# Kernel optimization log

Hardware: AMD Instinct MI355X
Metric: run time of the kernel (lower is better)

Reference implementation:

```python
import jax, jax.numpy as jnp
import numpy as np

IN_DIM, HIDDEN, OUT_DIM, BRANCH = 700, 1024, 20, 4
B, T = 128, 250
VTH = 1.0
WARMUP = 0
# surrogate-gradient constants (DH-SNN ActFun_adp); only used in backward
GAMMA, LENS, SCALE, HIGHT = 0.5, 0.5, 6.0, 0.15
SQRT2PI = float(np.sqrt(2.0 * np.pi))


def _gauss(x, mu, sigma):
    return jnp.exp(-((x - mu) ** 2) / (2.0 * sigma * sigma)) / (SQRT2PI * sigma)


@jax.custom_vjp
def spike_fn(x):
    # heaviside spike with multi-gaussian surrogate gradient
    return (x > 0).astype(x.dtype)


def _spike_fwd(x):
    return spike_fn(x), x


def _spike_bwd(x, g):
    temp = (_gauss(x, 0.0, LENS) * (1.0 + HIGHT)
            - _gauss(x, LENS, SCALE * LENS) * HIGHT
            - _gauss(x, -LENS, SCALE * LENS) * HIGHT)
    return (g * temp * GAMMA,)


spike_fn.defvjp(_spike_fwd, _spike_bwd)


def _branch_mask(rng):
    # each neuron's branch j sees a random disjoint slice of the (input+recurrent) fan-in
    isz = IN_DIM + HIDDEN
    seg = isz // BRANCH
    mask = np.zeros((HIDDEN * BRANCH, isz), np.float32)
    for i in range(HIDDEN):
        perm = rng.permutation(isz)
        for j in range(BRANCH):
            mask[i * BRANCH + j, perm[j * seg:(j + 1) * seg]] = 1.0
    return mask


def setup_inputs() -> dict:
    key = jax.random.key(0)
    ks = jax.random.split(key, 8)
    isz = IN_DIM + HIDDEN
    x = jax.random.normal(ks[0], (B, T, IN_DIM), jnp.float32)
    W = jax.random.normal(ks[1], (HIDDEN * BRANCH, isz), jnp.float32) / np.float32(np.sqrt(isz))
    W = W * jnp.asarray(_branch_mask(np.random.RandomState(0)))  # apply_mask() pre-applied
    b = jnp.zeros((HIDDEN * BRANCH,), jnp.float32)
    tau_m = jax.random.uniform(ks[2], (HIDDEN,), jnp.float32, 0.0, 4.0)
    tau_n = jax.random.uniform(ks[3], (HIDDEN, BRANCH), jnp.float32, 2.0, 6.0)  # low_n/high_n
    Wr = jax.random.normal(ks[4], (OUT_DIM, HIDDEN), jnp.float32) / np.float32(np.sqrt(HIDDEN))
    br = jnp.zeros((OUT_DIM,), jnp.float32)
    tau_r = jax.random.uniform(ks[5], (OUT_DIM,), jnp.float32, 0.0, 4.0)
    mem0 = jax.random.uniform(ks[6], (B, HIDDEN), jnp.float32) * VTH  # set_neuron_state: rand*vth
    return {"x": x, "W": W, "b": b, "tau_m": tau_m, "tau_n": tau_n,
            "Wr": Wr, "br": br, "tau_r": tau_r, "mem0": mem0}


def reference(x, W, b, tau_m, tau_n, Wr, br, tau_r, mem0):
    Bsz, Tlen = x.shape[0], x.shape[1]
    beta = jax.nn.sigmoid(tau_n)      # [H, BR] dendritic branch decay
    alpha = jax.nn.sigmoid(tau_m)     # [H]     soma decay
    alpha_r = jax.nn.sigmoid(tau_r)   # [O]     readout decay
    spike0 = jnp.zeros((Bsz, HIDDEN), x.dtype)
    d0 = jnp.zeros((Bsz, HIDDEN, BRANCH), x.dtype)
    rmem0 = jnp.zeros((Bsz, OUT_DIM), x.dtype)
    acc0 = jnp.zeros((Bsz, OUT_DIM), x.dtype)

    def step(carry, inp):
        mem, spk, d_in, rmem, acc = carry
        x_t, t = inp
        k = jnp.concatenate([x_t, spk], axis=1)                 # [B, in+H]
        cur = (k @ W.T + b).reshape(Bsz, HIDDEN, BRANCH)        # branch currents
        d_in = beta * d_in + (1.0 - beta) * cur                 # dendritic integration
        l_in = d_in.sum(axis=2)                                 # [B, H]
        mem = mem * alpha + (1.0 - alpha) * l_in - VTH * spk    # soma, soft reset (R_m=1)
        spk = spike_fn(mem - VTH)
        rmem = rmem * alpha_r + (1.0 - alpha_r) * (spk @ Wr.T + br)
        acc = acc + jnp.where(t > WARMUP, jax.nn.softmax(rmem, axis=1), 0.0)
        return (mem, spk, d_in, rmem, acc), None

    xs = (jnp.swapaxes(x, 0, 1), jnp.arange(Tlen))
    (_, _, _, _, acc), _ = jax.lax.scan(step, (mem0, spike0, d0, rmem0, acc0), xs)
    return acc
```

## Files before the change

### kernel.cpp

```cpp
#include <hip/hip_runtime.h>
#include <hip/hip_bf16.h>
#include <stdint.h>


typedef short short8 __attribute__((ext_vector_type(8)));
typedef float f32x4 __attribute__((ext_vector_type(4)));

#define T_STEPS 250
#define BATCH   128
#define HID     1024
#define NCOL    4096
#define IND     700
#define ISZ     1724
#define KPAD    704
#define OUTD    20
#define WGT     256
#define UPB     5632

#define O_P1F   0
#define O_SUM   4096
#define O_CHK   8192
#define O_WST   73728
#define O_WXH   16850944
#define O_XH    22618112

#define SM_BP    0
#define SM_A2    45568
#define SM_CURL2 135680
#define SM_MTB   144896
#define SM_TOTAL 153600

#define AGENT __HIP_MEMORY_SCOPE_AGENT

__device__ __forceinline__ float sigmoidf(float x) { return 1.0f / (1.0f + expf(-x)); }

__device__ __forceinline__ unsigned ldsLd(const unsigned* p) {
    return __hip_atomic_load(p, __ATOMIC_ACQUIRE, __HIP_MEMORY_SCOPE_WORKGROUP);
}
__device__ __forceinline__ void ldsSt(unsigned* p, unsigned v) {
    __hip_atomic_store(p, v, __ATOMIC_RELEASE, __HIP_MEMORY_SCOPE_WORKGROUP);
}

__device__ __forceinline__ void dma16(const void* g, void* l) {
    __builtin_amdgcn_global_load_lds(
        (const __attribute__((address_space(1))) unsigned int*)g,
        (__attribute__((address_space(3))) unsigned int*)l, 16, 0, 0);
}

__device__ __forceinline__ float qsum4(float v) {
    union { float f; int i; } a, b;
    a.f = v; b.i = __builtin_amdgcn_mov_dpp(a.i, 0xB1, 0xF, 0xF, true); v += b.f;
    a.f = v; b.i = __builtin_amdgcn_mov_dpp(a.i, 0x4E, 0xF, 0xF, true); v += b.f;
    return v;
}

__device__ __forceinline__ short bf16bits(float v) {
    union { __hip_bfloat16 h; short s; } u;
    u.h = __float2bfloat16(v);
    return u.s;
}

__global__ __launch_bounds__(256) void prep_all(
    const float* __restrict__ x, const float* __restrict__ W,
    __hip_bfloat16* __restrict__ Xh, __hip_bfloat16* __restrict__ Wxh,
    float* __restrict__ Wst, uint64_t* __restrict__ p1f,
    uint64_t* __restrict__ sums, uint64_t* __restrict__ chunks)
{
    const int bid = blockIdx.x;
    const int tid = threadIdx.x;

    if (bid < 2048) {
        const int total = T_STEPS * 2 * UPB;
        for (int unit = bid * 256 + tid; unit < total; unit += 2048 * 256) {
            int q    = unit % UPB;
            int blk  = unit / UPB;
            int half = blk & 1, t = blk >> 1;
            int row  = q / 88, m = q % 88;
            int k8   = m ^ (row & 7);
            int b    = half * 64 + row;
            int k0   = k8 * 8;
            const float* xp = x + ((long)b * T_STEPS + t) * IND + k0;
            short8 o;
            if (k0 + 8 <= IND) {
                f32x4 v0 = *(const f32x4*)xp;
                f32x4 v1 = *(const f32x4*)(xp + 4);
                #pragma unroll
                for (int e = 0; e < 4; ++e) { o[e] = bf16bits(v0[e]); o[4 + e] = bf16bits(v1[e]); }
            } else {
                #pragma unroll
                for (int e = 0; e < 8; ++e)
                    o[e] = bf16bits((k0 + e < IND) ? xp[e] : 0.0f);
            }
            *(short8*)(Xh + (size_t)unit * 8) = o;
        }
    } else if (bid < 4096) {
        if (bid == 2048) {
            for (int i = tid; i < 512; i += 256)
                __hip_atomic_store(&p1f[i], 0ull, __ATOMIC_RELAXED, AGENT);
            for (int i = tid; i < 2 * 2 * 128; i += 256)
                __hip_atomic_store(&sums[i], 0ull, __ATOMIC_RELAXED, AGENT);
            for (int i = tid; i < 2 * 2 * 128 * 16; i += 256)
                __hip_atomic_store(&chunks[i], 0ull, __ATOMIC_RELAXED, AGENT);
        }
        const int total = NCOL * 88;
        for (int unit = (bid - 2048) * 256 + tid; unit < total; unit += 2048 * 256) {
            int n = unit / 88, m = unit % 88;
            int k0 = m * 8;
            const float* wp = W + (long)n * ISZ + k0;
            short8 o;
            if (k0 + 8 <= IND) {
                f32x4 v0 = *(const f32x4*)wp;
                f32x4 v1 = *(const f32x4*)(wp + 4);
                #pragma unroll
                for (int e = 0; e < 4; ++e) { o[e] = bf16bits(v0[e]); o[4 + e] = bf16bits(v1[e]); }
            } else {
                #pragma unroll
                for (int e = 0; e < 8; ++e)
                    o[e] = bf16bits((k0 + e < IND) ? wp[e] : 0.0f);
            }
            *(short8*)(Wxh + (long)n * KPAD + k0) = o;
        }
    } else {
        __shared__ float tile[32][33];
        const int idx = bid - 4096;
        const int h0 = (idx & 31) * 32, n0 = (idx >> 5) * 32;
        const int tx = tid & 31, ty = tid >> 5;
        #pragma unroll
        for (int j = 0; j < 32; j += 8)
            tile[ty + j][tx] = W[(long)(n0 + ty + j) * ISZ + IND + h0 + tx];
        __syncthreads();
        #pragma unroll
        for (int j = 0; j < 32; j += 8)
            Wst[(long)(h0 + ty + j) * NCOL + n0 + tx] = tile[tx][ty + j];
    }
}

__global__ __launch_bounds__(256, 2) void p1_scan(
    const __hip_bfloat16* __restrict__ Xh, const __hip_bfloat16* __restrict__ Wxh,
    const float* __restrict__ bvec, const float* __restrict__ tau_m,
    const float* __restrict__ tau_n, const float* __restrict__ mem0,
    uint64_t* __restrict__ p1f)
{
    __shared__ __align__(16) uint8_t Abuf[2][22528];
    __shared__ __align__(16) float preg[2][8 * 256];
    __shared__ unsigned anySpkF;

    const int wg    = blockIdx.x;
    const int rtile = wg & 7;
    const int ctile = wg >> 3;
    const int tid   = threadIdx.x;
    const int lane  = tid & 63, wid = tid >> 6;
    const int colA  = lane & 15, kb8 = (lane >> 4) * 8;
    const int cg    = wid >> 1;
    const int p     = wid & 1;

    if (tid == 0) anySpkF = 0u;

    const int colG0 = ctile * 64 + cg * 32 + colA;
    const int colG1 = colG0 + 16;
    const int rowB  = rtile * 16 + (lane >> 4) * 4;
    float bt_[2], omb_[2], bias_[2], al_[2], oma_[2], dn[2][4], mem_[2][4];
    {
        const int cG[2] = {colG0, colG1};
        #pragma unroll
        for (int i = 0; i < 2; ++i) {
            bt_[i]   = sigmoidf(tau_n[cG[i]]);
            omb_[i]  = 1.0f - bt_[i];
            bias_[i] = bvec[cG[i]];
            al_[i]   = sigmoidf(tau_m[cG[i] >> 2]);
            oma_[i]  = 1.0f - al_[i];
            #pragma unroll
            for (int j = 0; j < 4; ++j) {
                dn[i][j]   = 0.0f;
                mem_[i][j] = mem0[(rowB + j) * HID + (cG[i] >> 2)];
            }
        }
    }

    short8 Breg[22];
    #pragma unroll
    for (int j = 0; j < 11; ++j) {
        Breg[2 * j]     = *(const short8*)(Wxh + (long)colG0 * KPAD + (11 * p + j) * 32 + kb8);
        Breg[2 * j + 1] = *(const short8*)(Wxh + (long)colG1 * KPAD + (11 * p + j) * 32 + kb8);
    }
    asm volatile("s_waitcnt vmcnt(0)" ::: "memory");
    __builtin_amdgcn_sched_barrier(0);
    #pragma unroll
    for (int i = 0; i < 22; ++i) asm volatile("" : "+v"(Breg[i]));

    const size_t sliceBase = (size_t)(rtile >> 2) * 90112 + (size_t)(rtile & 3) * 22528;
    const int dstart = (wid < 2) ? wid * 6 : 12 + (wid - 2) * 5;
    const int dcnt   = (wid < 2) ? 6 : 5;
    const char* XhB  = (const char*)Xh;

    #define ISSUE_A(T, BUF)                                                            \
        do {                                                                           \
            const char* _g = XhB + sliceBase + (size_t)(T) * 180224;                   \
            _Pragma("unroll")                                                          \
            for (int _i = 0; _i < 6; ++_i)                                             \
                if (_i < dcnt)                                                         \
                    dma16(_g + (size_t)(dstart + _i) * 1024 + (size_t)lane * 16,       \
                          (BUF) + (dstart + _i) * 1024);                               \
        } while (0)

    const int rl = lane & 15;
    const int sw = rl & 7;

    #define MFMA_BLOCK(AB, A0, A1)                                                             \
        do {                                                                                   \
            _Pragma("unroll")                                                                  \
            for (int _j = 0; _j < 11; ++_j) {                                                  \
                int _k8 = (11 * p + _j) * 4 + (lane >> 4);                                     \
                short8 _a = *(const short8*)((AB) + ((rl * 88 + (_k8 ^ sw)) << 4));            \
                A0 = __builtin_amdgcn_mfma_f32_16x16x32_bf16(_a, Breg[2 * _j],     A0, 0,0,0); \
                A1 = __builtin_amdgcn_mfma_f32_16x16x32_bf16(_a, Breg[2 * _j + 1], A1, 0,0,0); \
            }                                                                                  \
        } while (0)

    #define UPDATE_STEP(CS0, CS1)                                                  \
        do {                                                                       \
            _Pragma("unroll")                                                      \
            for (int _j = 0; _j < 4; ++_j) {                                       \
                float _d0 = bt_[0] * dn[0][_j] + omb_[0] * ((CS0)[_j] + bias_[0]); \
                float _d1 = bt_[1] * dn[1][_j] + omb_[1] * ((CS1)[_j] + bias_[1]); \
                dn[0][_j] = _d0; dn[1][_j] = _d1;                                  \
                float _l0 = qsum4(_d0), _l1 = qsum4(_d1);                          \
                float _m0 = al_[0] * mem_[0][_j] + oma_[0] * _l0;                  \
                float _m1 = al_[1] * mem_[1][_j] + oma_[1] * _l1;                  \
                mem_[0][_j] = _m0; mem_[1][_j] = _m1;                              \
                memmax = fmaxf(memmax, fmaxf(_m0, _m1));                           \
            }                                                                      \
        } while (0)

    float memmax = -1e30f;
    f32x4 own0, own1, prt0, prt1;
    const int wrSlot = (cg * 2 + (1 - p)) * 2;
    const int rdSlot = (cg * 2 + p) * 2;

    ISSUE_A(0, Abuf[0]);
    asm volatile("s_waitcnt vmcnt(0)" ::: "memory");
    __builtin_amdgcn_sched_barrier(0);
    __syncthreads();

    {
        ISSUE_A(1, Abuf[1]);
        f32x4 acc0 = {0,0,0,0}, acc1 = {0,0,0,0};
        MFMA_BLOCK(Abuf[0], acc0, acc1);
        float* wq = &preg[0][wrSlot * 256 + lane * 4];
        *(f32x4*)wq = acc0; *(f32x4*)(wq + 256) = acc1;
        asm volatile("s_waitcnt vmcnt(0) lgkmcnt(0)" ::: "memory");
        __builtin_amdgcn_sched_barrier(0);
        __builtin_amdgcn_s_barrier();
        const float* rq = &preg[0][rdSlot * 256 + lane * 4];
        prt0 = *(const f32x4*)rq; prt1 = *(const f32x4*)(rq + 256);
        own0 = acc0; own1 = acc1;
    }

    for (int t = 1; t < T_STEPS; ++t) {
        if (t + 1 < T_STEPS)
            ISSUE_A(t + 1, Abuf[(t + 1) & 1]);
        f32x4 acc0 = {0,0,0,0}, acc1 = {0,0,0,0};
        MFMA_BLOCK(Abuf[t & 1], acc0, acc1);
        {
            f32x4 cs0 = own0 + prt0;
            f32x4 cs1 = own1 + prt1;
            UPDATE_STEP(cs0, cs1);
        }
        float* wq = &preg[t & 1][wrSlot * 256 + lane * 4];
        *(f32x4*)wq = acc0; *(f32x4*)(wq + 256) = acc1;
        asm volatile("s_waitcnt vmcnt(0) lgkmcnt(0)" ::: "memory");
        __builtin_amdgcn_sched_barrier(0);
        __builtin_amdgcn_s_barrier();
        const float* rq = &preg[t & 1][rdSlot * 256 + lane * 4];
        prt0 = *(const f32x4*)rq; prt1 = *(const f32x4*)(rq + 256);
        own0 = acc0; own1 = acc1;
    }

    {
        f32x4 cs0 = own0 + prt0;
        f32x4 cs1 = own1 + prt1;
        UPDATE_STEP(cs0, cs1);
    }

    if (__any(memmax > 1.0f) && lane == 0) anySpkF = 1u;
    __syncthreads();
    if (tid == 0)
        __hip_atomic_store(p1f + wg, (1ull << 32) | (uint64_t)anySpkF,
                           __ATOMIC_RELAXED, AGENT);
    #undef ISSUE_A
    #undef MFMA_BLOCK
    #undef UPDATE_STEP
}

__global__ __launch_bounds__(256, 1) void p2_fallback(
    const __hip_bfloat16* __restrict__ Xh, const __hip_bfloat16* __restrict__ Wxh,
    const float* __restrict__ Wst, const uint64_t* __restrict__ p1f,
    uint64_t* __restrict__ sums, uint64_t* __restrict__ chunks,
    const float* __restrict__ bvec, const float* __restrict__ tau_m, const float* __restrict__ tau_n,
    const float* __restrict__ Wr, const float* __restrict__ brv, const float* __restrict__ tau_r,
    const float* __restrict__ mem0, float* __restrict__ out)
{
    __shared__ __align__(16) char smem[SM_TOTAL];
    __shared__ uint32_t stageW[16];
    __shared__ uint64_t roSnap[16];
    __shared__ unsigned fPollDone[2], fStgw[2], fCorr[2];
    __shared__ unsigned fRoSnap, dirtyH[2];

    __hip_bfloat16* Bp    = (__hip_bfloat16*)(smem + SM_BP);
    uint8_t*        Apre2 = (uint8_t*)(smem + SM_A2);
    float*          curL2 = (float*)(smem + SM_CURL2);
    uint8_t*        mTb   = (uint8_t*)(smem + SM_MTB);

    const int wg   = blockIdx.x;
    const int tid  = threadIdx.x;
    const int lane = tid & 63, wid = tid >> 6;
    const int colA = lane & 15, kb8 = (lane >> 4) * 8;

    if (tid < 2) { fPollDone[tid] = 0; fStgw[tid] = 0; fCorr[tid] = 0; dirtyH[tid] = 0; }
    if (tid == 0) fRoSnap = 0;
    __syncthreads();

    {
        uint64_t v0 = p1f[tid];
        uint64_t v1 = p1f[tid + 256];
        if ((unsigned)v0) dirtyH[(tid & 7) >> 2] = 1u;
        if ((unsigned)v1) dirtyH[((tid + 256) & 7) >> 2] = 1u;
    }
    __syncthreads();

    float r_alpha = 0.f, r_bias = 0.f;
    const float* WrRow = Wr;
    if (wid == 0 && lane < 32) {
        int o = (lane < OUTD) ? lane : 0;
        r_alpha = sigmoidf(tau_r[o]);
        r_bias  = brv[o];
        WrRow   = Wr + o * HID;
    }

    if (wg < BATCH && wid == 0 && lane < 32 && !dirtyH[wg >> 6]) {
        float rr = 0.f, racc = 0.f;
        for (int t = 0; t < T_STEPS; ++t) {
            rr = r_alpha * rr + (1.0f - r_alpha) * r_bias;
            float vmax = (lane < OUTD) ? rr : -__builtin_inff();
            #pragma unroll
            for (int d = 16; d > 0; d >>= 1) vmax = fmaxf(vmax, __shfl_xor(vmax, d, 32));
            float e = (lane < OUTD) ? expf(rr - vmax) : 0.f;
            float ss = e;
            #pragma unroll
            for (int d = 16; d > 0; d >>= 1) ss += __shfl_xor(ss, d, 32);
            if (t >= 1) racc += e / ss;
        }
        if (lane < OUTD) out[wg * OUTD + lane] = racc;
    }
    if (!dirtyH[wg >> 7]) return;

    float r_rmem = 0.f, r_acc = 0.f;
    const int w2    = wg & 127;
    const int bhalf = wg >> 7;
    const int bbase = bhalf * 64;
    const int c0    = w2 * 32;
    const int i0    = w2 * 8;
    const int roB2  = (wg < 64) ? wg : ((wg >= 128 && wg < 192) ? wg - 64 : -1);

    for (int idx = tid; idx < 32 * 88; idx += WGT) {
        int col = idx / 88, m = idx % 88;
        *(short8*)(Bp + col * 712 + m * 8) = *(const short8*)(Wxh + (long)(c0 + col) * KPAD + m * 8);
    }
    for (int idx = tid; idx < 64 * 136 / 4; idx += WGT)
        ((uint32_t*)mTb)[idx] = 0u;

    const int mwid = wid - 2;
    const int st   = tid - 128;
    const int r2   = st >> 1;
    const int half = st & 1;
    float dn2[16], bt2[16], omb2[16], bias2[16], alph2[4], oma2[4], mem2[4], spk2[4];
    if (wid >= 2) {
        const int b2 = bbase + r2;
        #pragma unroll
        for (int n = 0; n < 4; ++n) {
            int i = i0 + half * 4 + n;
            alph2[n] = sigmoidf(tau_m[i]);
            oma2[n]  = 1.0f - alph2[n];
            mem2[n]  = mem0[b2 * HID + i];
            spk2[n]  = 0.0f;
            #pragma unroll
            for (int j = 0; j < 4; ++j) {
                int idx = n * 4 + j;
                bt2[idx]   = sigmoidf(tau_n[i * 4 + j]);
                omb2[idx]  = 1.0f - bt2[idx];
                bias2[idx] = bvec[i * 4 + j];
                dn2[idx]   = 0.0f;
            }
        }
    }
    const int trRow = mwid * 32;
    const int rb2   = trRow + (lane & 15);
    const int sw2   = rb2 & 7;
    uint8_t* dst2   = Apre2 + mwid * 45056;

    if (wid >= 2) {
        const char* gsrc = (const char*)Xh + ((size_t)bhalf * UPB) * 16 + (size_t)mwid * 45056;
        #pragma unroll
        for (int i = 0; i < 44; ++i)
            dma16(gsrc + i * 1024 + lane * 16, dst2 + i * 1024);
    }
    asm volatile("s_waitcnt vmcnt(0)" ::: "memory");
    __syncthreads();

    if (wid < 2) {
        const int plane = tid;
        for (int k = 1; k <= T_STEPS; ++k) {
            const size_t base = ((size_t)((k - 1) & 1) * 2 + bhalf) * 128 + plane;
            const unsigned want = (unsigned)(k + 1);
            uint64_t v;
            for (;;) {
                v = __hip_atomic_load(sums + base, __ATOMIC_RELAXED, AGENT);
                if ((unsigned)(v >> 32) == want) break;
                __builtin_amdgcn_s_sleep(1);
            }
            unsigned mysum = (unsigned)v;
            if (mysum) {
                if (wid == 1)
                    while (ldsLd(&fRoSnap) < (unsigned)(k - 1)) {}
                const uint64_t* rec = chunks + base * 16;
                uint8_t* col = mTb + plane;
                unsigned pend = mysum;
                while (pend) {
                    int c = __builtin_ctz(pend);
                    uint64_t cv = __hip_atomic_load(rec + c, __ATOMIC_RELAXED, AGENT);
                    if ((unsigned)(cv >> 32) == want) {
                        pend &= pend - 1;
                        unsigned pay = (unsigned)cv;
                        col[(4 * c + 0) * 136] = (uint8_t)(pay);
                        col[(4 * c + 1) * 136] = (uint8_t)(pay >> 8);
                        col[(4 * c + 2) * 136] = (uint8_t)(pay >> 16);
                        col[(4 * c + 3) * 136] = (uint8_t)(pay >> 24);
                    } else {
                        __builtin_amdgcn_s_sleep(1);
                    }
                }
            }
            const bool anyW = __any(mysum != 0u);
            if (lane == 0)
                ldsSt(&fPollDone[wid], ((unsigned)k << 1) | (anyW ? 1u : 0u));

            if (wid == 0) {
                while ((ldsLd(&fPollDone[1]) >> 1) < (unsigned)k) {}
                if (roB2 >= 0 && lane < 16)
                    roSnap[lane] = ((const uint64_t*)(mTb + (roB2 & 63) * 136))[lane];
                asm volatile("s_waitcnt lgkmcnt(0)" ::: "memory");
                if (lane == 0) ldsSt(&fRoSnap, (unsigned)k);
                if (roB2 >= 0 && lane < 32) {
                    float rsum = 0.f;
                    #pragma unroll 4
                    for (int q = 0; q < 16; ++q) {
                        uint64_t mword = roSnap[q];
                        while (mword) {
                            int h = (q << 6) + __builtin_ctzll(mword);
                            mword &= mword - 1;
                            rsum += WrRow[h];
                        }
                    }
                    r_rmem = r_alpha * r_rmem + (1.0f - r_alpha) * (rsum + r_bias);
                    float vmax = (lane < OUTD) ? r_rmem : -__builtin_inff();
                    #pragma unroll
                    for (int d = 16; d > 0; d >>= 1) vmax = fmaxf(vmax, __shfl_xor(vmax, d, 32));
                    float e = (lane < OUTD) ? expf(r_rmem - vmax) : 0.f;
                    float ssum = e;
                    #pragma unroll
                    for (int d = 16; d > 0; d >>= 1) ssum += __shfl_xor(ssum, d, 32);
                    if (k >= 2) r_acc += e / ssum;
                }
            }
        }
        if (wid == 0 && roB2 >= 0 && lane < OUTD) out[roB2 * OUTD + lane] = r_acc;
    } else {
        const float* clp = curL2 + r2 * 36 + half * 16;
        for (int t = 0; t < T_STEPS; ++t) {
            f32x4 a00 = {0,0,0,0}, a01 = {0,0,0,0}, a10 = {0,0,0,0}, a11 = {0,0,0,0};
            #pragma unroll
            for (int k0 = 0; k0 < KPAD; k0 += 32) {
                int k8 = (k0 >> 3) + (lane >> 4);
                short8 f0 = *(const short8*)&Apre2[(((rb2)      * 88 + (k8 ^ sw2)) << 4)];
                short8 f1 = *(const short8*)&Apre2[(((rb2 + 16) * 88 + (k8 ^ sw2)) << 4)];
                short8 b0 = *(const short8*)(&Bp[(colA) * 712 + k0 + kb8]);
                short8 b1 = *(const short8*)(&Bp[(16 + colA) * 712 + k0 + kb8]);
                a00 = __builtin_amdgcn_mfma_f32_16x16x32_bf16(f0, b0, a00, 0, 0, 0);
                a01 = __builtin_amdgcn_mfma_f32_16x16x32_bf16(f0, b1, a01, 0, 0, 0);
                a10 = __builtin_amdgcn_mfma_f32_16x16x32_bf16(f1, b0, a10, 0, 0, 0);
                a11 = __builtin_amdgcn_mfma_f32_16x16x32_bf16(f1, b1, a11, 0, 0, 0);
            }
            asm volatile("s_waitcnt lgkmcnt(0)" ::: "memory");
            __builtin_amdgcn_sched_barrier(0);
            if (t + 1 < T_STEPS) {
                const char* gsrc = (const char*)Xh
                    + (((size_t)(t + 1) * 2 + bhalf) * UPB) * 16 + (size_t)mwid * 45056;
                #pragma unroll
                for (int i = 0; i < 44; ++i)
                    dma16(gsrc + i * 1024 + lane * 16, dst2 + i * 1024);
            }
            {
                const int crow0 = trRow + ((lane >> 4) << 2);
                #pragma unroll
                for (int j = 0; j < 4; ++j) {
                    curL2[(crow0 + j) * 36 + colA]           = a00[j];
                    curL2[(crow0 + j) * 36 + 16 + colA]      = a01[j];
                    curL2[(crow0 + 16 + j) * 36 + colA]      = a10[j];
                    curL2[(crow0 + 16 + j) * 36 + 16 + colA] = a11[j];
                }
            }
            asm volatile("s_waitcnt lgkmcnt(0)" ::: "memory");
            __builtin_amdgcn_sched_barrier(0);

            f32x4 cv0 = *(const f32x4*)(clp + 0);
            f32x4 cv1 = *(const f32x4*)(clp + 4);
            f32x4 cv2 = *(const f32x4*)(clp + 8);
            f32x4 cv3 = *(const f32x4*)(clp + 12);
            float cl[16];
            #pragma unroll
            for (int e = 0; e < 4; ++e) {
                cl[e] = cv0[e]; cl[4 + e] = cv1[e]; cl[8 + e] = cv2[e]; cl[12 + e] = cv3[e];
            }
            float memS[4], spkS[4];
            #pragma unroll
            for (int n = 0; n < 4; ++n) {
                float lin = 0.f;
                #pragma unroll
                for (int j = 0; j < 4; ++j) {
                    int idx = n * 4 + j;
                    dn2[idx] = bt2[idx] * dn2[idx] + omb2[idx] * (cl[idx] + bias2[idx]);
                    lin += dn2[idx];
                }
                memS[n] = alph2[n] * mem2[n] + oma2[n] * lin - spk2[n];
                spkS[n] = (memS[n] > 1.0f) ? 1.0f : 0.0f;
            }
            unsigned nib = 0;
            #pragma unroll
            for (int n = 0; n < 4; ++n) nib |= (spkS[n] != 0.f ? 1u : 0u) << (half * 4 + n);
            nib |= (unsigned)__shfl_xor((int)nib, 1);
            if (half == 0) ((uint8_t*)stageW)[r2] = (uint8_t)nib;
            if (lane == 0) ldsSt(&fStgw[mwid], (unsigned)(t + 1));

            bool anySpk = false;
            if (t > 0) {
                unsigned p0, p1;
                do { p0 = ldsLd(&fPollDone[0]); } while ((p0 >> 1) < (unsigned)t);
                do { p1 = ldsLd(&fPollDone[1]); } while ((p1 >> 1) < (unsigned)t);
                anySpk = ((p0 | p1) & 1u) != 0u;
            }
            if (anySpk) {
                float recv[16];
                #pragma unroll
                for (int e = 0; e < 16; ++e) recv[e] = 0.f;
                const float* Wb = Wst + c0 + half * 16;
                const uint64_t* mrow = (const uint64_t*)(mTb + r2 * 136);
                for (int q = 0; q < 16; ++q) {
                    uint64_t mword = mrow[q];
                    while (mword) {
                        int h = (q << 6) + __builtin_ctzll(mword);
                        mword &= mword - 1;
                        const f32x4* wv = (const f32x4*)(Wb + (long)h * NCOL);
                        f32x4 w0 = wv[0], w1 = wv[1], w2v = wv[2], w3 = wv[3];
                        #pragma unroll
                        for (int e = 0; e < 4; ++e) {
                            recv[e] += w0[e]; recv[4 + e] += w1[e];
                            recv[8 + e] += w2v[e]; recv[12 + e] += w3[e];
                        }
                    }
                }
                #pragma unroll
                for (int n = 0; n < 4; ++n) {
                    float cs = 0.f;
                    #pragma unroll
                    for (int j = 0; j < 4; ++j) {
                        int idx = n * 4 + j;
                        float ad = omb2[idx] * recv[idx];
                        dn2[idx] += ad; cs += ad;
                    }
                    memS[n] += oma2[n] * cs;
                    spkS[n] = (memS[n] > 1.0f) ? 1.0f : 0.0f;
                }
                unsigned nib2 = 0;
                #pragma unroll
                for (int n = 0; n < 4; ++n) nib2 |= (spkS[n] != 0.f ? 1u : 0u) << (half * 4 + n);
                nib2 |= (unsigned)__shfl_xor((int)nib2, 1);
                if (half == 0) ((uint8_t*)stageW)[r2] = (uint8_t)nib2;
                if (roB2 >= 0) while (ldsLd(&fRoSnap) < (unsigned)t) {}
                uint64_t* mz = (uint64_t*)(mTb + r2 * 136) + half * 8;
                #pragma unroll
                for (int e = 0; e < 8; ++e) mz[e] = 0;
                if (lane == 0) ldsSt(&fCorr[mwid], (unsigned)(t + 1));
            }
            #pragma unroll
            for (int n = 0; n < 4; ++n) { mem2[n] = memS[n]; spk2[n] = spkS[n]; }

            if (mwid == 0) {
                while (ldsLd(&fStgw[1]) < (unsigned)(t + 1)) {}
                if (anySpk) while (ldsLd(&fCorr[1]) < (unsigned)(t + 1)) {}
                unsigned pay = (lane < 16) ? stageW[lane] : 0u;
                const size_t pbase = ((size_t)(t & 1) * 2 + bhalf) * 128 + w2;
                if (lane < 16 && pay)
                    __hip_atomic_store(chunks + pbase * 16 + lane,
                                       ((uint64_t)(unsigned)(t + 2) << 32) | (uint64_t)pay,
                                       __ATOMIC_RELAXED, AGENT);
                uint64_t bal = __ballot(pay != 0u);
                if (lane == 0)
                    __hip_atomic_store(sums + pbase,
                                       ((uint64_t)(unsigned)(t + 2) << 32) | (uint64_t)(bal & 0xFFFFull),
                                       __ATOMIC_RELAXED, AGENT);
            }
            asm volatile("s_waitcnt vmcnt(0)" ::: "memory");
        }
    }
}

extern "C" void kernel_launch(void* const* d_in, const int* in_sizes, int n_in,
                              void* d_out, int out_size, void* d_ws, size_t ws_size,
                              hipStream_t stream) {
    (void)in_sizes; (void)n_in; (void)out_size; (void)ws_size;
    const float* x     = (const float*)d_in[0];
    const float* W     = (const float*)d_in[1];
    const float* bv    = (const float*)d_in[2];
    const float* tau_m = (const float*)d_in[3];
    const float* tau_n = (const float*)d_in[4];
    const float* Wr    = (const float*)d_in[5];
    const float* br    = (const float*)d_in[6];
    const float* tau_r = (const float*)d_in[7];
    const float* mem0  = (const float*)d_in[8];

    char* ws = (char*)d_ws;
    uint64_t*        p1flag = (uint64_t*)(ws + O_P1F);
    uint64_t*        sums   = (uint64_t*)(ws + O_SUM);
    uint64_t*        chunks = (uint64_t*)(ws + O_CHK);
    float*           Wst    = (float*)(ws + O_WST);
    __hip_bfloat16*  Wxh    = (__hip_bfloat16*)(ws + O_WXH);
    __hip_bfloat16*  Xh     = (__hip_bfloat16*)(ws + O_XH);

    prep_all<<<8192, 256, 0, stream>>>(x, W, Xh, Wxh, Wst, p1flag, sums, chunks);
    p1_scan<<<512, WGT, 0, stream>>>(Xh, Wxh, bv, tau_m, tau_n, mem0, p1flag);
    p2_fallback<<<256, WGT, 0, stream>>>(Xh, Wxh, Wst, p1flag, sums, chunks,
                                         bv, tau_m, tau_n, Wr, br, tau_r, mem0, (float*)d_out);
}
```

Measured before the change: 385.0 us.

## Store bf16 input in MFMA fragment order and load A directly into registers

The prep kernel now writes the bf16 copy of x in a layout grouped by 16-row groups in MFMA-fragment order, so each lane's A operand is one contiguous 16-byte load. The p1 scan kernel drops its LDS double buffer and DMA staging and loads A fragments from global memory into registers, double-buffered across two unrolled half-steps. The fallback kernel's LDS staging and addressing are adapted to the new layout. This removes LDS traffic and XOR swizzle arithmetic from the scan's inner loop, but adds 22 extra short8 registers per lane and exposes global load latency more directly.

```diff
diff --git a/kernel.cpp b/kernel.cpp
--- a/kernel.cpp
+++ b/kernel.cpp
@@ -15,7 +15,8 @@
 #define KPAD    704
 #define OUTD    20
 #define WGT     256
-#define UPB     5632
+#define TSTRIDE 180224
+#define RGB     22528
 
 #define O_P1F   0
 #define O_SUM   4096
@@ -70,15 +71,17 @@
     const int tid = threadIdx.x;
 
     if (bid < 2048) {
-        const int total = T_STEPS * 2 * UPB;
-        for (int unit = bid * 256 + tid; unit < total; unit += 2048 * 256) {
-            int q    = unit % UPB;
-            int blk  = unit / UPB;
-            int half = blk & 1, t = blk >> 1;
-            int row  = q / 88, m = q % 88;
-            int k8   = m ^ (row & 7);
-            int b    = half * 64 + row;
-            int k0   = k8 * 8;
+        const int total = T_STEPS * 8 * 1408;
+        for (int u = bid * 256 + tid; u < total; u += 2048 * 256) {
+            int t   = u / 11264;
+            int rem = u % 11264;
+            int rg  = rem / 1408;
+            int v   = rem % 1408;
+            int c   = v >> 6;
+            int w   = v & 63;
+            int q   = w >> 4, rl = w & 15;
+            int b   = rg * 16 + rl;
+            int k0  = (c * 4 + q) * 8;
             const float* xp = x + ((long)b * T_STEPS + t) * IND + k0;
             short8 o;
             if (k0 + 8 <= IND) {
@@ -91,7 +94,7 @@
                 for (int e = 0; e < 8; ++e)
                     o[e] = bf16bits((k0 + e < IND) ? xp[e] : 0.0f);
             }
-            *(short8*)(Xh + (size_t)unit * 8) = o;
+            *(short8*)(Xh + (size_t)u * 8) = o;
         }
     } else if (bid < 4096) {
         if (bid == 2048) {
@@ -141,7 +144,6 @@
     const float* __restrict__ tau_n, const float* __restrict__ mem0,
     uint64_t* __restrict__ p1f)
 {
-    __shared__ __align__(16) uint8_t Abuf[2][22528];
     __shared__ __align__(16) float preg[2][8 * 256];
     __shared__ unsigned anySpkF;
 
@@ -188,32 +190,23 @@
     #pragma unroll
     for (int i = 0; i < 22; ++i) asm volatile("" : "+v"(Breg[i]));
 
-    const size_t sliceBase = (size_t)(rtile >> 2) * 90112 + (size_t)(rtile & 3) * 22528;
-    const int dstart = (wid < 2) ? wid * 6 : 12 + (wid - 2) * 5;
-    const int dcnt   = (wid < 2) ? 6 : 5;
-    const char* XhB  = (const char*)Xh;
-
-    #define ISSUE_A(T, BUF)                                                            \
-        do {                                                                           \
-            const char* _g = XhB + sliceBase + (size_t)(T) * 180224;                   \
-            _Pragma("unroll")                                                          \
-            for (int _i = 0; _i < 6; ++_i)                                             \
-                if (_i < dcnt)                                                         \
-                    dma16(_g + (size_t)(dstart + _i) * 1024 + (size_t)lane * 16,       \
-                          (BUF) + (dstart + _i) * 1024);                               \
+    const char* Abase = (const char*)Xh + (size_t)rtile * RGB + (size_t)(11 * p) * 1024
+                        + (size_t)lane * 16;
+
+    #define LOADA(T, A)                                                        \
+        do {                                                                   \
+            const char* _g = Abase + (size_t)(T) * TSTRIDE;                    \
+            _Pragma("unroll")                                                  \
+            for (int _j = 0; _j < 11; ++_j)                                    \
+                (A)[_j] = *(const short8*)(_g + _j * 1024);                    \
         } while (0)
 
-    const int rl = lane & 15;
-    const int sw = rl & 7;
-
-    #define MFMA_BLOCK(AB, A0, A1)                                                             \
+    #define MFMA_R(A, a0, a1)                                                                  \
         do {                                                                                   \
             _Pragma("unroll")                                                                  \
             for (int _j = 0; _j < 11; ++_j) {                                                  \
-                int _k8 = (11 * p + _j) * 4 + (lane >> 4);                                     \
-                short8 _a = *(const short8*)((AB) + ((rl * 88 + (_k8 ^ sw)) << 4));            \
-                A0 = __builtin_amdgcn_mfma_f32_16x16x32_bf16(_a, Breg[2 * _j],     A0, 0,0,0); \
-                A1 = __builtin_amdgcn_mfma_f32_16x16x32_bf16(_a, Breg[2 * _j + 1], A1, 0,0,0); \
+                a0 = __builtin_amdgcn_mfma_f32_16x16x32_bf16((A)[_j], Breg[2 * _j],     a0, 0,0,0); \
+                a1 = __builtin_amdgcn_mfma_f32_16x16x32_bf16((A)[_j], Breg[2 * _j + 1], a1, 0,0,0); \
             }                                                                                  \
         } while (0)
 
@@ -232,50 +225,42 @@
             }                                                                      \
         } while (0)
 
+    #define HALF(S, ACUR, ANEXT, DO_LOAD, DO_UPD)                              \
+        do {                                                                   \
+            if (DO_LOAD) { LOADA((S) + 1, ANEXT); }                            \
+            __builtin_amdgcn_sched_barrier(0);                                 \
+            f32x4 _a0 = {0,0,0,0}, _a1 = {0,0,0,0};                            \
+            MFMA_R(ACUR, _a0, _a1);                                            \
+            if (DO_UPD) {                                                      \
+                f32x4 _cs0 = own0 + prt0;                                      \
+                f32x4 _cs1 = own1 + prt1;                                      \
+                UPDATE_STEP(_cs0, _cs1);                                       \
+            }                                                                  \
+            float* _wq = &preg[(S) & 1][wrSlot * 256 + lane * 4];              \
+            *(f32x4*)_wq = _a0; *(f32x4*)(_wq + 256) = _a1;                    \
+            asm volatile("s_waitcnt lgkmcnt(0)" ::: "memory");                 \
+            __builtin_amdgcn_sched_barrier(0);                                 \
+            __builtin_amdgcn_s_barrier();                                      \
+            const float* _rq = &preg[(S) & 1][rdSlot * 256 + lane * 4];        \
+            prt0 = *(const f32x4*)_rq; prt1 = *(const f32x4*)(_rq + 256);      \
+            own0 = _a0; own1 = _a1;                                            \
+        } while (0)
+
     float memmax = -1e30f;
     f32x4 own0, own1, prt0, prt1;
     const int wrSlot = (cg * 2 + (1 - p)) * 2;
     const int rdSlot = (cg * 2 + p) * 2;
 
-    ISSUE_A(0, Abuf[0]);
-    asm volatile("s_waitcnt vmcnt(0)" ::: "memory");
-    __builtin_amdgcn_sched_barrier(0);
+    short8 A0[11], A1[11];
+    LOADA(0, A0);
     __syncthreads();
 
-    {
-        ISSUE_A(1, Abuf[1]);
-        f32x4 acc0 = {0,0,0,0}, acc1 = {0,0,0,0};
-        MFMA_BLOCK(Abuf[0], acc0, acc1);
-        float* wq = &preg[0][wrSlot * 256 + lane * 4];
-        *(f32x4*)wq = acc0; *(f32x4*)(wq + 256) = acc1;
-        asm volatile("s_waitcnt vmcnt(0) lgkmcnt(0)" ::: "memory");
-        __builtin_amdgcn_sched_barrier(0);
-        __builtin_amdgcn_s_barrier();
-        const float* rq = &preg[0][rdSlot * 256 + lane * 4];
-        prt0 = *(const f32x4*)rq; prt1 = *(const f32x4*)(rq + 256);
-        own0 = acc0; own1 = acc1;
-    }
-
-    for (int t = 1; t < T_STEPS; ++t) {
-        if (t + 1 < T_STEPS)
-            ISSUE_A(t + 1, Abuf[(t + 1) & 1]);
-        f32x4 acc0 = {0,0,0,0}, acc1 = {0,0,0,0};
-        MFMA_BLOCK(Abuf[t & 1], acc0, acc1);
-        {
-            f32x4 cs0 = own0 + prt0;
-            f32x4 cs1 = own1 + prt1;
-            UPDATE_STEP(cs0, cs1);
-        }
-        float* wq = &preg[t & 1][wrSlot * 256 + lane * 4];
-        *(f32x4*)wq = acc0; *(f32x4*)(wq + 256) = acc1;
-        asm volatile("s_waitcnt vmcnt(0) lgkmcnt(0)" ::: "memory");
-        __builtin_amdgcn_sched_barrier(0);
-        __builtin_amdgcn_s_barrier();
-        const float* rq = &preg[t & 1][rdSlot * 256 + lane * 4];
-        prt0 = *(const f32x4*)rq; prt1 = *(const f32x4*)(rq + 256);
-        own0 = acc0; own1 = acc1;
-    }
-
+    HALF(0, A0, A1, true, false);
+    for (int t = 1; t < 249; t += 2) {
+        HALF(t,     A1, A0, true, true);
+        HALF(t + 1, A0, A1, true, true);
+    }
+    HALF(249, A1, A0, false, true);
     {
         f32x4 cs0 = own0 + prt0;
         f32x4 cs1 = own1 + prt1;
@@ -287,9 +272,10 @@
     if (tid == 0)
         __hip_atomic_store(p1f + wg, (1ull << 32) | (uint64_t)anySpkF,
                            __ATOMIC_RELAXED, AGENT);
-    #undef ISSUE_A
-    #undef MFMA_BLOCK
+    #undef LOADA
+    #undef MFMA_R
     #undef UPDATE_STEP
+    #undef HALF
 }
 
 __global__ __launch_bounds__(256, 1) void p2_fallback(
@@ -395,15 +381,22 @@
     }
     const int trRow = mwid * 32;
     const int rb2   = trRow + (lane & 15);
-    const int sw2   = rb2 & 7;
     uint8_t* dst2   = Apre2 + mwid * 45056;
-
-    if (wid >= 2) {
-        const char* gsrc = (const char*)Xh + ((size_t)bhalf * UPB) * 16 + (size_t)mwid * 45056;
-        #pragma unroll
-        for (int i = 0; i < 44; ++i)
-            dma16(gsrc + i * 1024 + lane * 16, dst2 + i * 1024);
-    }
+    const int rg0   = bhalf * 4 + mwid * 2;
+
+    #define P2_STAGE(T)                                                               \
+        do {                                                                          \
+            _Pragma("unroll")                                                         \
+            for (int _g = 0; _g < 2; ++_g) {                                          \
+                const char* _src = (const char*)Xh + ((size_t)(T) * 8 + rg0 + _g) * RGB; \
+                _Pragma("unroll")                                                     \
+                for (int _i = 0; _i < 22; ++_i)                                       \
+                    dma16(_src + _i * 1024 + (size_t)lane * 16,                       \
+                          dst2 + _g * RGB + _i * 1024);                               \
+            }                                                                         \
+        } while (0)
+
+    if (wid >= 2) P2_STAGE(0);
     asm volatile("s_waitcnt vmcnt(0)" ::: "memory");
     __syncthreads();
 
@@ -480,9 +473,12 @@
             f32x4 a00 = {0,0,0,0}, a01 = {0,0,0,0}, a10 = {0,0,0,0}, a11 = {0,0,0,0};
             #pragma unroll
             for (int k0 = 0; k0 < KPAD; k0 += 32) {
-                int k8 = (k0 >> 3) + (lane >> 4);
-                short8 f0 = *(const short8*)&Apre2[(((rb2)      * 88 + (k8 ^ sw2)) << 4)];
-                short8 f1 = *(const short8*)&Apre2[(((rb2 + 16) * 88 + (k8 ^ sw2)) << 4)];
+                int c  = k0 >> 5;
+                int q  = lane >> 4;
+                int rl = rb2 & 15;
+                const uint8_t* ab = Apre2 + (rb2 >> 4) * RGB + c * 1024 + q * 256 + rl * 16;
+                short8 f0 = *(const short8*)(ab);
+                short8 f1 = *(const short8*)(ab + RGB);
                 short8 b0 = *(const short8*)(&Bp[(colA) * 712 + k0 + kb8]);
                 short8 b1 = *(const short8*)(&Bp[(16 + colA) * 712 + k0 + kb8]);
                 a00 = __builtin_amdgcn_mfma_f32_16x16x32_bf16(f0, b0, a00, 0, 0, 0);
@@ -492,13 +488,7 @@
             }
             asm volatile("s_waitcnt lgkmcnt(0)" ::: "memory");
             __builtin_amdgcn_sched_barrier(0);
-            if (t + 1 < T_STEPS) {
-                const char* gsrc = (const char*)Xh
-                    + (((size_t)(t + 1) * 2 + bhalf) * UPB) * 16 + (size_t)mwid * 45056;
-                #pragma unroll
-                for (int i = 0; i < 44; ++i)
-                    dma16(gsrc + i * 1024 + lane * 16, dst2 + i * 1024);
-            }
+            if (t + 1 < T_STEPS) P2_STAGE(t + 1);
             {
                 const int crow0 = trRow + ((lane >> 4) << 2);
                 #pragma unroll
@@ -543,10 +533,10 @@
 
             bool anySpk = false;
             if (t > 0) {
-                unsigned p0, p1;
+                unsigned p0, p1v;
                 do { p0 = ldsLd(&fPollDone[0]); } while ((p0 >> 1) < (unsigned)t);
-                do { p1 = ldsLd(&fPollDone[1]); } while ((p1 >> 1) < (unsigned)t);
-                anySpk = ((p0 | p1) & 1u) != 0u;
+                do { p1v = ldsLd(&fPollDone[1]); } while ((p1v >> 1) < (unsigned)t);
+                anySpk = ((p0 | p1v) & 1u) != 0u;
             }
             if (anySpk) {
                 float recv[16];
@@ -612,6 +602,7 @@
             asm volatile("s_waitcnt vmcnt(0)" ::: "memory");
         }
     }
+    #undef P2_STAGE
 }
 
 extern "C" void kernel_launch(void* const* d_in, const int* in_sizes, int n_in,
```

New measurement: 374.8 us. -2.7%, faster.
